# Kernel optimization log

Hardware: AMD Instinct MI355X
Metric: run time of the kernel (lower is better)

The kernel has to match this reference:

```python
import jax, jax.numpy as jnp
import numpy as np
import math

N = 32768
NUM_BATCH = 64
DIM_QK = 128
DIM_V = 256
M_FEATURES = 256
EPS_PHI = 1e-4
EPS_NORM = 1e-8


def _make_omega(nrows, ncols, rng):
    """Block-orthogonal random feature matrix, faithful to Attention._omega.
    Returns [ncols, nrows] (i.e. [dim_qk, m])."""
    nblocks = nrows // ncols
    blocks = []
    for _ in range(nblocks):
        q, _ = np.linalg.qr(rng.normal(size=(ncols, ncols)))
        blocks.append(q.T)
    missing = nrows - nblocks * ncols
    if missing > 0:
        q, _ = np.linalg.qr(rng.normal(size=(ncols, ncols)))
        blocks.append(q.T[:missing])
    norm = np.linalg.norm(rng.normal(size=(nrows, ncols)), axis=1, keepdims=True)
    return (norm * np.vstack(blocks)).T.astype(np.float32)


def setup_inputs() -> dict:
    key = jax.random.key(0)
    kq, kk, kv = jax.random.split(key, 3)
    Q = jax.random.normal(kq, (N, DIM_QK), dtype=jnp.float32)
    K = jax.random.normal(kk, (N, DIM_QK), dtype=jnp.float32)
    V = jax.random.normal(kv, (N, DIM_V), dtype=jnp.float32)
    # contiguous equal-size segments (64 molecules x 512 atoms)
    batch_seg = jnp.repeat(jnp.arange(NUM_BATCH, dtype=jnp.int32), N // NUM_BATCH)
    omega = jnp.asarray(_make_omega(M_FEATURES, DIM_QK, np.random.default_rng(0)))
    return {"Q": Q, "K": K, "V": V, "omega": omega,
            "num_batch": NUM_BATCH, "batch_seg": batch_seg}


def reference(Q, K, V, omega, num_batch, batch_seg):
    d = Q.shape[-1]
    m = omega.shape[-1]
    inv_sqrt_m = 1.0 / math.sqrt(m)

    def phi(X, is_query):
        U = (X / d ** 0.25) @ omega                       # [N, m]
        h = jnp.sum(X * X, axis=-1, keepdims=True) / (2.0 * d ** 0.5)
        if is_query:
            mx = jnp.max(U, axis=-1, keepdims=True)       # per-row max
        else:
            # per-segment max over all rows & features, gathered back per row
            seg_max = jax.ops.segment_max(jnp.max(U, axis=-1), batch_seg,
                                          num_segments=num_batch)
            mx = seg_max[batch_seg][:, None]
        return (jnp.exp(U - h - mx) + EPS_PHI) * inv_sqrt_m

    Qp = phi(Q, True)    # [N, m]
    Kp = phi(K, False)   # [N, m]

    # normalizer: Qp . (sum of Kp within segment)
    Ksum = jax.ops.segment_sum(Kp, batch_seg, num_segments=num_batch)  # [B, m]
    norm = jnp.sum(Qp * Ksum[batch_seg], axis=-1, keepdims=True) + EPS_NORM

    # Linear-attention equivalent of (mask * (Kp @ Qp^T))^T @ V:
    # out[i] = Qp[i] @ sum_{j in seg(i)} Kp[j] V[j]^T. Segments are
    # contiguous & equal-sized, so segment reductions become batched einsums.
    n_per = Q.shape[0] // num_batch
    Kpb = Kp.reshape(num_batch, n_per, m)
    Vb = V.reshape(num_batch, n_per, -1)
    KV = jnp.einsum('bnm,bnv->bmv', Kpb, Vb)              # [B, m, dv]
    Qpb = Qp.reshape(num_batch, n_per, m)
    out = jnp.einsum('bnm,bmv->bnv', Qpb, KV).reshape(Q.shape[0], -1)
    return out / norm
```

## Files before the change

### kernel.cpp

```cpp
#include <hip/hip_runtime.h>
#include <math.h>

#define NTOT 32768
#define NB   64
#define NPB  512
#define DQK  128
#define MF   256
#define DVV  256

#define QK_SCALE   0.29730177875068026f
#define INV_SQRT_M 0.0625f
#define EPS_PHI    1e-4f
#define EPS_NORM   1e-8f
#define EPS_ISM    (EPS_PHI * INV_SQRT_M)

typedef float f32x4  __attribute__((ext_vector_type(4)));
typedef short bf16x8 __attribute__((ext_vector_type(8)));
typedef unsigned short us4 __attribute__((ext_vector_type(4)));
typedef unsigned short us8 __attribute__((ext_vector_type(8)));

static __device__ __forceinline__ float red_max32(float v) {
    v = fmaxf(v, __shfl_xor(v, 1, 64));
    v = fmaxf(v, __shfl_xor(v, 2, 64));
    v = fmaxf(v, __shfl_xor(v, 4, 64));
    v = fmaxf(v, __shfl_xor(v, 8, 64));
    v = fmaxf(v, __shfl_xor(v, 16, 64));
    return v;
}
static __device__ __forceinline__ float red_sum32(float v) {
    v += __shfl_xor(v, 1, 64);
    v += __shfl_xor(v, 2, 64);
    v += __shfl_xor(v, 4, 64);
    v += __shfl_xor(v, 8, 64);
    v += __shfl_xor(v, 16, 64);
    return v;
}
static __device__ __forceinline__ float red_sum16(float v) {
    v += __shfl_xor(v, 1, 64);
    v += __shfl_xor(v, 2, 64);
    v += __shfl_xor(v, 4, 64);
    v += __shfl_xor(v, 8, 64);
    return v;
}
static __device__ __forceinline__ float red_max16(float v) {
    v = fmaxf(v, __shfl_xor(v, 1, 64));
    v = fmaxf(v, __shfl_xor(v, 2, 64));
    v = fmaxf(v, __shfl_xor(v, 4, 64));
    v = fmaxf(v, __shfl_xor(v, 8, 64));
    return v;
}

static __device__ __forceinline__ void bfsplit(float x, unsigned short& h, unsigned short& l) {
    unsigned u = __float_as_uint(x);
    unsigned r = (u + 0x7fffu + ((u >> 16) & 1u)) & 0xffff0000u;
    h = (unsigned short)(r >> 16);
    float lo = x - __uint_as_float(r);
    unsigned v = __float_as_uint(lo);
    l = (unsigned short)((v + 0x7fffu + ((v >> 16) & 1u)) >> 16);
}

__global__ __launch_bounds__(256) void omsplit_kernel(
    const float* __restrict__ omega,
    unsigned short* __restrict__ OmTh, unsigned short* __restrict__ OmTl)
{
    const int k = blockIdx.x;
    const int m = threadIdx.x;
    unsigned short h, l;
    bfsplit(omega[k * MF + m], h, l);
    OmTh[(size_t)m * DQK + k] = h;
    OmTl[(size_t)m * DQK + k] = l;
}

template <bool IS_QUERY>
__global__ __launch_bounds__(256) void phi_kernel(
    const float* __restrict__ X,
    const unsigned short* __restrict__ OmTh, const unsigned short* __restrict__ OmTl,
    const float* __restrict__ Ksum,
    float* __restrict__ out, float* __restrict__ aux)
{
    __shared__ __align__(16) float Xf[64][132];
    __shared__ float hS[64];
    __shared__ float mxW[4][64];
    __shared__ float npW[4][64];
    __shared__ float KsS[256];

    const int tid  = threadIdx.x;
    const int lane = tid & 63;
    const int w    = tid >> 6;
    const int fr   = lane & 15;
    const int k8   = (lane >> 4) * 8;
    const int rg   = (lane >> 4) * 4;
    const int row0 = blockIdx.x * 64;

    if (IS_QUERY) KsS[tid] = Ksum[(row0 >> 9) * MF + tid];

    float hp[8];
    {
        const float4* Xv = (const float4*)(X + (size_t)row0 * DQK);
        #pragma unroll
        for (int j = 0; j < 8; ++j) {
            int idx = tid + 256 * j;
            int r = idx >> 5, c4 = idx & 31;
            float4 v = Xv[idx];
            v.x *= QK_SCALE; v.y *= QK_SCALE; v.z *= QK_SCALE; v.w *= QK_SCALE;
            *(float4*)&Xf[r][c4 * 4] = v;
            hp[j] = v.x * v.x + v.y * v.y + v.z * v.z + v.w * v.w;
        }
    }
    __syncthreads();
    #pragma unroll
    for (int j = 0; j < 8; ++j) hp[j] = red_sum32(hp[j]);
    if ((tid & 31) == 0) {
        #pragma unroll
        for (int j = 0; j < 8; ++j) hS[(tid >> 5) + 8 * j] = hp[j];
    }

    f32x4 acc[4][4] = {};
    #pragma unroll
    for (int c = 0; c < 4; ++c) {
        bf16x8 ah[4], al[4];
        #pragma unroll
        for (int t = 0; t < 4; ++t) {
            float a[8];
            *(float4*)&a[0] = *(const float4*)&Xf[t * 16 + fr][c * 32 + k8];
            *(float4*)&a[4] = *(const float4*)&Xf[t * 16 + fr][c * 32 + k8 + 4];
            unsigned short hh[8], ll[8];
            #pragma unroll
            for (int s = 0; s < 8; ++s) bfsplit(a[s], hh[s], ll[s]);
            ah[t] = *(bf16x8*)&hh[0];
            al[t] = *(bf16x8*)&ll[0];
        }
        #pragma unroll
        for (int u = 0; u < 4; ++u) {
            const size_t ob = (size_t)(w * 64 + u * 16 + fr) * DQK + c * 32 + k8;
            bf16x8 bh = *(const bf16x8*)&OmTh[ob];
            bf16x8 bl = *(const bf16x8*)&OmTl[ob];
            #pragma unroll
            for (int t = 0; t < 4; ++t) {
                acc[t][u] = __builtin_amdgcn_mfma_f32_16x16x32_bf16(ah[t], bh, acc[t][u], 0, 0, 0);
                acc[t][u] = __builtin_amdgcn_mfma_f32_16x16x32_bf16(ah[t], bl, acc[t][u], 0, 0, 0);
                acc[t][u] = __builtin_amdgcn_mfma_f32_16x16x32_bf16(al[t], bh, acc[t][u], 0, 0, 0);
            }
        }
    }

    #pragma unroll
    for (int t = 0; t < 4; ++t) {
        #pragma unroll
        for (int g = 0; g < 4; ++g) {
            float m0 = fmaxf(fmaxf(acc[t][0][g], acc[t][1][g]),
                             fmaxf(acc[t][2][g], acc[t][3][g]));
            m0 = red_max16(m0);
            if (fr == 0) mxW[w][t * 16 + rg + g] = m0;
        }
    }
    __syncthreads();

    #pragma unroll
    for (int t = 0; t < 4; ++t) {
        #pragma unroll
        for (int g = 0; g < 4; ++g) {
            const int row  = t * 16 + rg + g;
            const int grow = row0 + row;
            const float mxa = fmaxf(fmaxf(mxW[0][row], mxW[1][row]),
                                    fmaxf(mxW[2][row], mxW[3][row]));
            const float hm = 0.5f * hS[row] + mxa;
            if (IS_QUERY) {
                float np = 0.f;
                #pragma unroll
                for (int u = 0; u < 4; ++u) {
                    const int col = w * 64 + u * 16 + fr;
                    const float q = (__expf(acc[t][u][g] - hm) + EPS_PHI) * INV_SQRT_M;
                    out[(size_t)grow * MF + col] = q;
                    np = fmaf(q, KsS[col], np);
                }
                np = red_sum16(np);
                if (fr == 0) npW[w][row] = np;
            } else {
                #pragma unroll
                for (int u = 0; u < 4; ++u)
                    out[(size_t)grow * MF + w * 64 + u * 16 + fr] = __expf(acc[t][u][g] - hm);
                if (w == 0 && fr == 0) aux[grow] = mxa;
            }
        }
    }
    if (IS_QUERY) {
        __syncthreads();
        if (w == 0 && fr == 0) {
            #pragma unroll
            for (int t = 0; t < 4; ++t)
                #pragma unroll
                for (int g = 0; g < 4; ++g) {
                    const int row = t * 16 + rg + g;
                    aux[row0 + row] = npW[0][row] + npW[1][row] + npW[2][row] + npW[3][row];
                }
        }
    }
}

__global__ __launch_bounds__(256) void segsexp_kernel(
    const float* __restrict__ rmax, float* __restrict__ sexp)
{
    const int b = blockIdx.x, tid = threadIdx.x;
    const float r0 = rmax[b * NPB + tid];
    const float r1 = rmax[b * NPB + 256 + tid];
    float v = fmaxf(r0, r1);
    v = red_max32(v);
    v = fmaxf(v, __shfl_xor(v, 32, 64));
    __shared__ float red[4];
    if ((tid & 63) == 0) red[tid >> 6] = v;
    __syncthreads();
    const float smax = fmaxf(fmaxf(red[0], red[1]), fmaxf(red[2], red[3]));
    sexp[b * NPB + tid]       = __expf(r0 - smax);
    sexp[b * NPB + 256 + tid] = __expf(r1 - smax);
}

__global__ __launch_bounds__(256) void kv_kernel(
    const float* __restrict__ A, const float* __restrict__ V,
    const float* __restrict__ sexp,
    float* __restrict__ KV, float* __restrict__ P1,
    float* __restrict__ P2, float* __restrict__ P3,
    float* __restrict__ Ksum, float* __restrict__ KsumP)
{
    __shared__ __align__(16) float Af[32][132];
    __shared__ __align__(16) float Vf[32][132];
    __shared__ __align__(16) unsigned short KpH[128][40];
    __shared__ __align__(16) unsigned short KpL[128][40];
    __shared__ __align__(16) unsigned short VH[128][40];
    __shared__ __align__(16) unsigned short VL[128][40];

    const int tid  = threadIdx.x;
    const int lane = tid & 63;
    const int w    = tid >> 6;
    const int wr   = w >> 1;
    const int wc   = w & 1;
    const int fr   = lane & 15;
    const int k8   = (lane >> 4) * 8;
    const int rg   = (lane >> 4) * 4;

    const int vt = blockIdx.x, mt = blockIdx.y;
    const int b  = blockIdx.z >> 2, ch = blockIdx.z & 3;
    const int m0 = mt * 128, v0 = vt * 128;
    const size_t n0 = (size_t)b * NPB + ch * 128;

    const int ln  = tid >> 5;
    const int lm4 = tid & 31;
    const int tv  = tid >> 1;
    const int th  = tid & 1;

    f32x4 acc[4][4] = {};
    float4 ks4 = {0.f, 0.f, 0.f, 0.f};

    for (int c = 0; c < 4; ++c) {
        __syncthreads();
        #pragma unroll
        for (int j = 0; j < 4; ++j) {
            const size_t n = n0 + c * 32 + ln + 8 * j;
            float4 a  = *(const float4*)&A[n * MF + m0 + lm4 * 4];
            float4 vv = *(const float4*)&V[n * DVV + v0 + lm4 * 4];
            const float s2 = sexp[n] * INV_SQRT_M;
            float4 e;
            e.x = fmaf(a.x, s2, EPS_ISM);
            e.y = fmaf(a.y, s2, EPS_ISM);
            e.z = fmaf(a.z, s2, EPS_ISM);
            e.w = fmaf(a.w, s2, EPS_ISM);
            ks4.x += e.x; ks4.y += e.y; ks4.z += e.z; ks4.w += e.w;
            *(float4*)&Af[ln + 8 * j][lm4 * 4] = e;
            *(float4*)&Vf[ln + 8 * j][lm4 * 4] = vv;
        }
        __syncthreads();
        {
            unsigned short hh[16], ll[16];
            #pragma unroll
            for (int s = 0; s < 16; ++s)
                bfsplit(Af[th * 16 + s][tv], hh[s], ll[s]);
            *(us8*)&KpH[tv][th * 16]     = *(us8*)&hh[0];
            *(us8*)&KpH[tv][th * 16 + 8] = *(us8*)&hh[8];
            *(us8*)&KpL[tv][th * 16]     = *(us8*)&ll[0];
            *(us8*)&KpL[tv][th * 16 + 8] = *(us8*)&ll[8];
            #pragma unroll
            for (int s = 0; s < 16; ++s)
                bfsplit(Vf[th * 16 + s][tv], hh[s], ll[s]);
            *(us8*)&VH[tv][th * 16]     = *(us8*)&hh[0];
            *(us8*)&VH[tv][th * 16 + 8] = *(us8*)&hh[8];
            *(us8*)&VL[tv][th * 16]     = *(us8*)&ll[0];
            *(us8*)&VL[tv][th * 16 + 8] = *(us8*)&ll[8];
        }
        __syncthreads();
        bf16x8 ah[4], al[4];
        #pragma unroll
        for (int t = 0; t < 4; ++t) {
            ah[t] = *(const bf16x8*)&KpH[wr * 64 + t * 16 + fr][k8];
            al[t] = *(const bf16x8*)&KpL[wr * 64 + t * 16 + fr][k8];
        }
        #pragma unroll
        for (int u = 0; u < 4; ++u) {
            bf16x8 bh = *(const bf16x8*)&VH[wc * 64 + u * 16 + fr][k8];
            bf16x8 bl = *(const bf16x8*)&VL[wc * 64 + u * 16 + fr][k8];
            #pragma unroll
            for (int t = 0; t < 4; ++t) {
                acc[t][u] = __builtin_amdgcn_mfma_f32_16x16x32_bf16(ah[t], bh, acc[t][u], 0, 0, 0);
                acc[t][u] = __builtin_amdgcn_mfma_f32_16x16x32_bf16(ah[t], bl, acc[t][u], 0, 0, 0);
                acc[t][u] = __builtin_amdgcn_mfma_f32_16x16x32_bf16(al[t], bh, acc[t][u], 0, 0, 0);
            }
        }
    }

    float* __restrict__ dKV = (ch == 0) ? KV : (ch == 1) ? P1 : (ch == 2) ? P2 : P3;
    #pragma unroll
    for (int t = 0; t < 4; ++t) {
        #pragma unroll
        for (int g = 0; g < 4; ++g) {
            const int row = wr * 64 + t * 16 + rg + g;
            const size_t base = ((size_t)b * MF + m0 + row) * DVV + v0 + wc * 64;
            #pragma unroll
            for (int u = 0; u < 4; ++u)
                dKV[base + u * 16 + fr] = acc[t][u][g];
        }
    }

    if (vt == 0) {
        __syncthreads();
        float* scr = &Af[0][0];
        *(float4*)&scr[(ln * 32 + lm4) * 4] = ks4;
        __syncthreads();
        if (tid < 128) {
            float s = 0.f;
            #pragma unroll
            for (int g = 0; g < 8; ++g) s += scr[g * 128 + tid];
            float* dst = (ch == 0) ? (Ksum + b * MF)
                                   : (KsumP + ((ch - 1) * NB + b) * MF);
            dst[m0 + tid] = s;
        }
    }
}

__global__ __launch_bounds__(256) void kvreduce_kernel(
    float* __restrict__ KV, const float* __restrict__ P1,
    const float* __restrict__ P2, const float* __restrict__ P3,
    float* __restrict__ Ksum, const float* __restrict__ KsumP)
{
    const int idx = blockIdx.x * 256 + threadIdx.x;
    const int stride = gridDim.x * 256;
    const int TOT4 = NB * MF * DVV / 4;
    for (int i = idx; i < TOT4; i += stride) {
        float4 a  = ((const float4*)KV)[i];
        float4 p1 = ((const float4*)P1)[i];
        float4 p2 = ((const float4*)P2)[i];
        float4 p3 = ((const float4*)P3)[i];
        a.x += p1.x + p2.x + p3.x;
        a.y += p1.y + p2.y + p3.y;
        a.z += p1.z + p2.z + p3.z;
        a.w += p1.w + p2.w + p3.w;
        ((float4*)KV)[i] = a;
    }
    const int KS4 = NB * MF / 4;
    for (int i = idx; i < KS4; i += stride) {
        float4 a  = ((const float4*)Ksum)[i];
        float4 p1 = ((const float4*)KsumP)[i];
        float4 p2 = ((const float4*)KsumP)[i + KS4];
        float4 p3 = ((const float4*)KsumP)[i + 2 * KS4];
        a.x += p1.x + p2.x + p3.x;
        a.y += p1.y + p2.y + p3.y;
        a.z += p1.z + p2.z + p3.z;
        a.w += p1.w + p2.w + p3.w;
        ((float4*)Ksum)[i] = a;
    }
}

__global__ __launch_bounds__(256) void out_kernel(
    const float* __restrict__ Qp, const float* __restrict__ KVm,
    const float* __restrict__ normv, float* __restrict__ out)
{
    __shared__ __align__(16) unsigned short Qh[128][40];
    __shared__ __align__(16) unsigned short Ql[128][40];
    __shared__ __align__(16) unsigned short Kh[128][40];
    __shared__ __align__(16) unsigned short Kl[128][40];
    __shared__ __align__(16) float Kf[32][132];
    __shared__ float nrmS[128];

    const int tid  = threadIdx.x;
    const int lane = tid & 63;
    const int w    = tid >> 6;
    const int wr   = w >> 1;
    const int wc   = w & 1;
    const int fr   = lane & 15;
    const int k8   = (lane >> 4) * 8;

    const int vt = blockIdx.x, rt = blockIdx.y, b = blockIdx.z;
    const int v0 = vt * 128;
    const int r0 = b * NPB + rt * 128;

    if (tid < 128) nrmS[tid] = normv[r0 + tid];

    const int qr  = tid >> 3;
    const int qm4 = tid & 7;
    const int km  = tid >> 5;
    const int kv4 = tid & 31;
    const int tv  = tid >> 1;
    const int th  = tid & 1;

    f32x4 acc[4][4] = {};

    for (int c = 0; c < 8; ++c) {
        const int mc = c * 32;
        __syncthreads();
        #pragma unroll
        for (int j = 0; j < 4; ++j) {
            float4 q = *(const float4*)&Qp[(size_t)(r0 + qr + 32 * j) * MF + mc + qm4 * 4];
            unsigned short h0, l0, h1, l1, h2, l2, h3, l3;
            bfsplit(q.x, h0, l0); bfsplit(q.y, h1, l1);
            bfsplit(q.z, h2, l2); bfsplit(q.w, h3, l3);
            us4 hv = {h0, h1, h2, h3};
            us4 lv = {l0, l1, l2, l3};
            *(us4*)&Qh[qr + 32 * j][qm4 * 4] = hv;
            *(us4*)&Ql[qr + 32 * j][qm4 * 4] = lv;

            *(float4*)&Kf[km + 8 * j][kv4 * 4] =
                *(const float4*)&KVm[((size_t)b * MF + mc + km + 8 * j) * DVV + v0 + kv4 * 4];
        }
        __syncthreads();
        {
            unsigned short hh[16], ll[16];
            #pragma unroll
            for (int s = 0; s < 16; ++s)
                bfsplit(Kf[th * 16 + s][tv], hh[s], ll[s]);
            *(us8*)&Kh[tv][th * 16]     = *(us8*)&hh[0];
            *(us8*)&Kh[tv][th * 16 + 8] = *(us8*)&hh[8];
            *(us8*)&Kl[tv][th * 16]     = *(us8*)&ll[0];
            *(us8*)&Kl[tv][th * 16 + 8] = *(us8*)&ll[8];
        }
        __syncthreads();
        bf16x8 ah[4], al[4];
        #pragma unroll
        for (int t = 0; t < 4; ++t) {
            ah[t] = *(const bf16x8*)&Qh[wr * 64 + t * 16 + fr][k8];
            al[t] = *(const bf16x8*)&Ql[wr * 64 + t * 16 + fr][k8];
        }
        #pragma unroll
        for (int u = 0; u < 4; ++u) {
            bf16x8 bh = *(const bf16x8*)&Kh[wc * 64 + u * 16 + fr][k8];
            bf16x8 bl = *(const bf16x8*)&Kl[wc * 64 + u * 16 + fr][k8];
            #pragma unroll
            for (int t = 0; t < 4; ++t) {
                acc[t][u] = __builtin_amdgcn_mfma_f32_16x16x32_bf16(ah[t], bh, acc[t][u], 0, 0, 0);
                acc[t][u] = __builtin_amdgcn_mfma_f32_16x16x32_bf16(ah[t], bl, acc[t][u], 0, 0, 0);
                acc[t][u] = __builtin_amdgcn_mfma_f32_16x16x32_bf16(al[t], bh, acc[t][u], 0, 0, 0);
            }
        }
    }

    const int rg = (lane >> 4) * 4;
    #pragma unroll
    for (int t = 0; t < 4; ++t) {
        #pragma unroll
        for (int g = 0; g < 4; ++g) {
            const int row = wr * 64 + t * 16 + rg + g;
            const float inv = 1.0f / (nrmS[row] + EPS_NORM);
            const size_t base = (size_t)(r0 + row) * DVV + v0 + wc * 64;
            #pragma unroll
            for (int u = 0; u < 4; ++u)
                out[base + u * 16 + fr] = acc[t][u][g] * inv;
        }
    }
}

extern "C" void kernel_launch(void* const* d_in, const int* in_sizes, int n_in,
                              void* d_out, int out_size, void* d_ws, size_t ws_size,
                              hipStream_t stream)
{
    const float* Q     = (const float*)d_in[0];
    const float* K     = (const float*)d_in[1];
    const float* V     = (const float*)d_in[2];
    const float* omega = (const float*)d_in[3];
    float* out = (float*)d_out;

    float* ws    = (float*)d_ws;
    float* Qp    = ws;
    float* A     = Qp    + (size_t)NTOT * MF;
    float* KV    = A     + (size_t)NTOT * MF;
    float* Ksum  = KV    + (size_t)NB * MF * DVV;
    float* KsumP = Ksum  + (size_t)NB * MF;
    float* rmaxA = KsumP + (size_t)3 * NB * MF;
    float* sexp  = rmaxA + NTOT;
    float* normv = sexp  + NTOT;
    unsigned short* OmTh = (unsigned short*)(normv + NTOT);
    unsigned short* OmTl = OmTh + (size_t)MF * DQK;

    float* P1 = Qp;
    float* P2 = Qp + (size_t)NB * MF * DVV;
    float* P3 = out;

    omsplit_kernel<<<DQK, 256, 0, stream>>>(omega, OmTh, OmTl);
    phi_kernel<false><<<NTOT / 64, 256, 0, stream>>>(K, OmTh, OmTl, (const float*)nullptr, A, rmaxA);
    segsexp_kernel<<<NB, 256, 0, stream>>>(rmaxA, sexp);
    kv_kernel<<<dim3(2, 2, NB * 4), 256, 0, stream>>>(A, V, sexp, KV, P1, P2, P3, Ksum, KsumP);
    kvreduce_kernel<<<2048, 256, 0, stream>>>(KV, P1, P2, P3, Ksum, KsumP);
    phi_kernel<true ><<<NTOT / 64, 256, 0, stream>>>(Q, OmTh, OmTl, Ksum, Qp, normv);
    out_kernel<<<dim3(2, 4, NB), 256, 0, stream>>>(Qp, KV, normv, out);
}
```

Measured before the change: 222.6 us.

## Pre-split Qp to bf16 hi/lo, fragment-order omega, halve KV split-K partials

The query phi kernel now writes Qp as bf16 hi/lo pairs, so out_kernel loads ready-made halves instead of reading fp32 and splitting them. Omega is stored in MFMA fragment order so each lane's B operand load is contiguous. The KV kernel splits the 512 rows into 2 chunks instead of 4, which cuts the partial buffers the reduce kernel has to read and sum, in exchange for fewer blocks and longer loops per block.

```diff
diff --git a/kernel.cpp b/kernel.cpp
--- a/kernel.cpp
+++ b/kernel.cpp
@@ -27,14 +27,6 @@
     v = fmaxf(v, __shfl_xor(v, 16, 64));
     return v;
 }
-static __device__ __forceinline__ float red_sum32(float v) {
-    v += __shfl_xor(v, 1, 64);
-    v += __shfl_xor(v, 2, 64);
-    v += __shfl_xor(v, 4, 64);
-    v += __shfl_xor(v, 8, 64);
-    v += __shfl_xor(v, 16, 64);
-    return v;
-}
 static __device__ __forceinline__ float red_sum16(float v) {
     v += __shfl_xor(v, 1, 64);
     v += __shfl_xor(v, 2, 64);
@@ -61,22 +53,28 @@
 
 __global__ __launch_bounds__(256) void omsplit_kernel(
     const float* __restrict__ omega,
-    unsigned short* __restrict__ OmTh, unsigned short* __restrict__ OmTl)
+    unsigned short* __restrict__ OmFh, unsigned short* __restrict__ OmFl)
 {
     const int k = blockIdx.x;
     const int m = threadIdx.x;
     unsigned short h, l;
     bfsplit(omega[k * MF + m], h, l);
-    OmTh[(size_t)m * DQK + k] = h;
-    OmTl[(size_t)m * DQK + k] = l;
+    const int M16 = m >> 4, fr = m & 15;
+    const int c = k >> 5, kk = k & 31;
+    const int lane = fr + 16 * (kk >> 3);
+    const size_t idx = ((size_t)(M16 * 4 + c) * 64 + lane) * 8 + (kk & 7);
+    OmFh[idx] = h;
+    OmFl[idx] = l;
 }
 
 template <bool IS_QUERY>
 __global__ __launch_bounds__(256) void phi_kernel(
     const float* __restrict__ X,
-    const unsigned short* __restrict__ OmTh, const unsigned short* __restrict__ OmTl,
+    const unsigned short* __restrict__ OmFh, const unsigned short* __restrict__ OmFl,
     const float* __restrict__ Ksum,
-    float* __restrict__ out, float* __restrict__ aux)
+    float* __restrict__ outF,
+    unsigned short* __restrict__ outH, unsigned short* __restrict__ outL,
+    float* __restrict__ aux)
 {
     __shared__ __align__(16) float Xf[64][132];
     __shared__ float hS[64];
@@ -109,7 +107,13 @@
     }
     __syncthreads();
     #pragma unroll
-    for (int j = 0; j < 8; ++j) hp[j] = red_sum32(hp[j]);
+    for (int j = 0; j < 8; ++j) {
+        hp[j] += __shfl_xor(hp[j], 1, 64);
+        hp[j] += __shfl_xor(hp[j], 2, 64);
+        hp[j] += __shfl_xor(hp[j], 4, 64);
+        hp[j] += __shfl_xor(hp[j], 8, 64);
+        hp[j] += __shfl_xor(hp[j], 16, 64);
+    }
     if ((tid & 31) == 0) {
         #pragma unroll
         for (int j = 0; j < 8; ++j) hS[(tid >> 5) + 8 * j] = hp[j];
@@ -132,9 +136,9 @@
         }
         #pragma unroll
         for (int u = 0; u < 4; ++u) {
-            const size_t ob = (size_t)(w * 64 + u * 16 + fr) * DQK + c * 32 + k8;
-            bf16x8 bh = *(const bf16x8*)&OmTh[ob];
-            bf16x8 bl = *(const bf16x8*)&OmTl[ob];
+            const size_t ob = ((size_t)((w * 4 + u) * 4 + c) * 64 + lane) * 8;
+            bf16x8 bh = *(const bf16x8*)&OmFh[ob];
+            bf16x8 bl = *(const bf16x8*)&OmFl[ob];
             #pragma unroll
             for (int t = 0; t < 4; ++t) {
                 acc[t][u] = __builtin_amdgcn_mfma_f32_16x16x32_bf16(ah[t], bh, acc[t][u], 0, 0, 0);
@@ -171,7 +175,10 @@
                 for (int u = 0; u < 4; ++u) {
                     const int col = w * 64 + u * 16 + fr;
                     const float q = (__expf(acc[t][u][g] - hm) + EPS_PHI) * INV_SQRT_M;
-                    out[(size_t)grow * MF + col] = q;
+                    unsigned short qh, ql;
+                    bfsplit(q, qh, ql);
+                    outH[(size_t)grow * MF + col] = qh;
+                    outL[(size_t)grow * MF + col] = ql;
                     np = fmaf(q, KsS[col], np);
                 }
                 np = red_sum16(np);
@@ -179,7 +186,7 @@
             } else {
                 #pragma unroll
                 for (int u = 0; u < 4; ++u)
-                    out[(size_t)grow * MF + w * 64 + u * 16 + fr] = __expf(acc[t][u][g] - hm);
+                    outF[(size_t)grow * MF + w * 64 + u * 16 + fr] = __expf(acc[t][u][g] - hm);
                 if (w == 0 && fr == 0) aux[grow] = mxa;
             }
         }
@@ -219,7 +226,6 @@
     const float* __restrict__ A, const float* __restrict__ V,
     const float* __restrict__ sexp,
     float* __restrict__ KV, float* __restrict__ P1,
-    float* __restrict__ P2, float* __restrict__ P3,
     float* __restrict__ Ksum, float* __restrict__ KsumP)
 {
     __shared__ __align__(16) float Af[32][132];
@@ -239,9 +245,9 @@
     const int rg   = (lane >> 4) * 4;
 
     const int vt = blockIdx.x, mt = blockIdx.y;
-    const int b  = blockIdx.z >> 2, ch = blockIdx.z & 3;
+    const int b  = blockIdx.z >> 1, ch = blockIdx.z & 1;
     const int m0 = mt * 128, v0 = vt * 128;
-    const size_t n0 = (size_t)b * NPB + ch * 128;
+    const size_t n0 = (size_t)b * NPB + ch * 256;
 
     const int ln  = tid >> 5;
     const int lm4 = tid & 31;
@@ -251,7 +257,7 @@
     f32x4 acc[4][4] = {};
     float4 ks4 = {0.f, 0.f, 0.f, 0.f};
 
-    for (int c = 0; c < 4; ++c) {
+    for (int c = 0; c < 8; ++c) {
         __syncthreads();
         #pragma unroll
         for (int j = 0; j < 4; ++j) {
@@ -306,7 +312,7 @@
         }
     }
 
-    float* __restrict__ dKV = (ch == 0) ? KV : (ch == 1) ? P1 : (ch == 2) ? P2 : P3;
+    float* __restrict__ dKV = ch ? P1 : KV;
     #pragma unroll
     for (int t = 0; t < 4; ++t) {
         #pragma unroll
@@ -328,48 +334,36 @@
             float s = 0.f;
             #pragma unroll
             for (int g = 0; g < 8; ++g) s += scr[g * 128 + tid];
-            float* dst = (ch == 0) ? (Ksum + b * MF)
-                                   : (KsumP + ((ch - 1) * NB + b) * MF);
-            dst[m0 + tid] = s;
+            (ch ? KsumP : Ksum)[b * MF + m0 + tid] = s;
         }
     }
 }
 
 __global__ __launch_bounds__(256) void kvreduce_kernel(
     float* __restrict__ KV, const float* __restrict__ P1,
-    const float* __restrict__ P2, const float* __restrict__ P3,
     float* __restrict__ Ksum, const float* __restrict__ KsumP)
 {
     const int idx = blockIdx.x * 256 + threadIdx.x;
     const int stride = gridDim.x * 256;
     const int TOT4 = NB * MF * DVV / 4;
     for (int i = idx; i < TOT4; i += stride) {
-        float4 a  = ((const float4*)KV)[i];
-        float4 p1 = ((const float4*)P1)[i];
-        float4 p2 = ((const float4*)P2)[i];
-        float4 p3 = ((const float4*)P3)[i];
-        a.x += p1.x + p2.x + p3.x;
-        a.y += p1.y + p2.y + p3.y;
-        a.z += p1.z + p2.z + p3.z;
-        a.w += p1.w + p2.w + p3.w;
+        float4 a = ((const float4*)KV)[i];
+        float4 p = ((const float4*)P1)[i];
+        a.x += p.x; a.y += p.y; a.z += p.z; a.w += p.w;
         ((float4*)KV)[i] = a;
     }
     const int KS4 = NB * MF / 4;
     for (int i = idx; i < KS4; i += stride) {
-        float4 a  = ((const float4*)Ksum)[i];
-        float4 p1 = ((const float4*)KsumP)[i];
-        float4 p2 = ((const float4*)KsumP)[i + KS4];
-        float4 p3 = ((const float4*)KsumP)[i + 2 * KS4];
-        a.x += p1.x + p2.x + p3.x;
-        a.y += p1.y + p2.y + p3.y;
-        a.z += p1.z + p2.z + p3.z;
-        a.w += p1.w + p2.w + p3.w;
+        float4 a = ((const float4*)Ksum)[i];
+        float4 p = ((const float4*)KsumP)[i];
+        a.x += p.x; a.y += p.y; a.z += p.z; a.w += p.w;
         ((float4*)Ksum)[i] = a;
     }
 }
 
 __global__ __launch_bounds__(256) void out_kernel(
-    const float* __restrict__ Qp, const float* __restrict__ KVm,
+    const unsigned short* __restrict__ QpH, const unsigned short* __restrict__ QpL,
+    const float* __restrict__ KVm,
     const float* __restrict__ normv, float* __restrict__ out)
 {
     __shared__ __align__(16) unsigned short Qh[128][40];
@@ -407,15 +401,9 @@
         __syncthreads();
         #pragma unroll
         for (int j = 0; j < 4; ++j) {
-            float4 q = *(const float4*)&Qp[(size_t)(r0 + qr + 32 * j) * MF + mc + qm4 * 4];
-            unsigned short h0, l0, h1, l1, h2, l2, h3, l3;
-            bfsplit(q.x, h0, l0); bfsplit(q.y, h1, l1);
-            bfsplit(q.z, h2, l2); bfsplit(q.w, h3, l3);
-            us4 hv = {h0, h1, h2, h3};
-            us4 lv = {l0, l1, l2, l3};
-            *(us4*)&Qh[qr + 32 * j][qm4 * 4] = hv;
-            *(us4*)&Ql[qr + 32 * j][qm4 * 4] = lv;
-
+            const size_t qb = (size_t)(r0 + qr + 32 * j) * MF + mc + qm4 * 4;
+            *(us4*)&Qh[qr + 32 * j][qm4 * 4] = *(const us4*)&QpH[qb];
+            *(us4*)&Ql[qr + 32 * j][qm4 * 4] = *(const us4*)&QpL[qb];
             *(float4*)&Kf[km + 8 * j][kv4 * 4] =
                 *(const float4*)&KVm[((size_t)b * MF + mc + km + 8 * j) * DVV + v0 + kv4 * 4];
         }
@@ -481,21 +469,23 @@
     float* KV    = A     + (size_t)NTOT * MF;
     float* Ksum  = KV    + (size_t)NB * MF * DVV;
     float* KsumP = Ksum  + (size_t)NB * MF;
-    float* rmaxA = KsumP + (size_t)3 * NB * MF;
+    float* rmaxA = KsumP + (size_t)NB * MF;
     float* sexp  = rmaxA + NTOT;
     float* normv = sexp  + NTOT;
-    unsigned short* OmTh = (unsigned short*)(normv + NTOT);
-    unsigned short* OmTl = OmTh + (size_t)MF * DQK;
+    unsigned short* OmFh = (unsigned short*)(normv + NTOT);
+    unsigned short* OmFl = OmFh + (size_t)MF * DQK;
 
     float* P1 = Qp;
-    float* P2 = Qp + (size_t)NB * MF * DVV;
-    float* P3 = out;
-
-    omsplit_kernel<<<DQK, 256, 0, stream>>>(omega, OmTh, OmTl);
-    phi_kernel<false><<<NTOT / 64, 256, 0, stream>>>(K, OmTh, OmTl, (const float*)nullptr, A, rmaxA);
+    unsigned short* QpH = (unsigned short*)Qp;
+    unsigned short* QpL = QpH + (size_t)NTOT * MF;
+
+    omsplit_kernel<<<DQK, 256, 0, stream>>>(omega, OmFh, OmFl);
+    phi_kernel<false><<<NTOT / 64, 256, 0, stream>>>(K, OmFh, OmFl, (const float*)nullptr,
+                                                     A, (unsigned short*)nullptr, (unsigned short*)nullptr, rmaxA);
     segsexp_kernel<<<NB, 256, 0, stream>>>(rmaxA, sexp);
-    kv_kernel<<<dim3(2, 2, NB * 4), 256, 0, stream>>>(A, V, sexp, KV, P1, P2, P3, Ksum, KsumP);
-    kvreduce_kernel<<<2048, 256, 0, stream>>>(KV, P1, P2, P3, Ksum, KsumP);
-    phi_kernel<true ><<<NTOT / 64, 256, 0, stream>>>(Q, OmTh, OmTl, Ksum, Qp, normv);
-    out_kernel<<<dim3(2, 4, NB), 256, 0, stream>>>(Qp, KV, normv, out);
-}
+    kv_kernel<<<dim3(2, 2, NB * 2), 256, 0, stream>>>(A, V, sexp, KV, P1, Ksum, KsumP);
+    kvreduce_kernel<<<2048, 256, 0, stream>>>(KV, P1, Ksum, KsumP);
+    phi_kernel<true ><<<NTOT / 64, 256, 0, stream>>>(Q, OmFh, OmFl, Ksum,
+                                                     (float*)nullptr, QpH, QpL, normv);
+    out_kernel<<<dim3(2, 4, NB), 256, 0, stream>>>(QpH, QpL, KV, normv, out);
+}
```

Measured after the change: 211.2 us. -5.1%, faster.
